# Performance work log

Hardware: AMD Instinct MI355X
Metric: run time of the kernel (lower is better)

Reference implementation:

```python
import jax, jax.numpy as jnp
import numpy as np

EPS = 1e-05


def setup_inputs() -> dict:
    key = jax.random.key(0)
    k1, k2, k3 = jax.random.split(key, 3)
    b, s, n, m = 16, 4096, 1024, 1024
    x = jax.random.normal(k1, (b, s, n), dtype=jnp.float32)
    # torch.rand -> uniform [0,1)
    A = jax.random.uniform(k2, (m, n), dtype=jnp.float32)
    B = jax.random.uniform(k3, (m, n), dtype=jnp.float32)
    return {"x": x, "A": A, "B": B}


def reference(x, A, B):
    # query: project each token with A, then sum over seq -> [b, m]
    query = jnp.einsum('ij,bsj->bi', A, x)  # fused projection + seq-sum
    query = query / (EPS + jnp.linalg.norm(query, axis=1, keepdims=True))
    # keys: [b, s, m], L2-normalized per token
    keys = jnp.einsum('ij,bsj->bsi', B, x)
    keys = keys / (EPS + jnp.linalg.norm(keys, axis=2, keepdims=True))
    # cosine-style similarity (no softmax): [b, s]
    sim = jnp.einsum('bi,bsi->bs', query, keys)
    # weighted sum of raw inputs: [b, n]
    out = jnp.einsum('bs,bsn->bn', sim, x)
    return (out, sim)
```

## Files before the change

kernel.cpp:

```cpp
#include <hip/hip_runtime.h>

#define EPS 1e-5f

typedef __bf16 bf16x8 __attribute__((ext_vector_type(8)));
typedef __bf16 bf16x4 __attribute__((ext_vector_type(4)));
typedef __bf16 bf16x2 __attribute__((ext_vector_type(2)));
typedef float f32x4 __attribute__((ext_vector_type(4)));

static __device__ __forceinline__ unsigned int f2bf(float f) {
    unsigned int u = __builtin_bit_cast(unsigned int, f);
    u = (u + 0x7fffu + ((u >> 16) & 1u)) >> 16;
    return u;
}

static __device__ __forceinline__ void gll16(const void* g, void* l) {
    __builtin_amdgcn_global_load_lds(
        (const __attribute__((address_space(1))) unsigned int*)(unsigned long long)g,
        (__attribute__((address_space(3))) unsigned int*)(unsigned int)(unsigned long long)l,
        16, 0, 0);
}

template <int XBF>
__global__ __launch_bounds__(256) void k_prep(const float* __restrict__ x,
                                              float* __restrict__ xs_part,
                                              unsigned short* __restrict__ xbf) {
    const int b = blockIdx.y, sc = blockIdx.x, tid = threadIdx.x;
    const size_t rowbase = ((size_t)(b * 4096 + sc * 128)) * 1024;
    const float4* src = (const float4*)(x + rowbase) + tid;
    uint2* dst = XBF ? ((uint2*)(xbf + rowbase) + tid) : (uint2*)0;
    float ax = 0.f, ay = 0.f, az = 0.f, aw = 0.f;
    for (int r = 0; r < 128; ++r) {
        float4 v = src[r * 256];
        ax += v.x; ay += v.y; az += v.z; aw += v.w;
        if (XBF) {
            uint2 p;
            p.x = f2bf(v.x) | (f2bf(v.y) << 16);
            p.y = f2bf(v.z) | (f2bf(v.w) << 16);
            dst[r * 256] = p;
        }
    }
    float4 o; o.x = ax; o.y = ay; o.z = az; o.w = aw;
    ((float4*)(xs_part + ((size_t)(b * 32 + sc)) * 1024))[tid] = o;
}

__global__ void k_bconv(const float* __restrict__ B, unsigned short* __restrict__ Bb) {
    const int i = blockIdx.x * 256 + threadIdx.x;
    float4 v = ((const float4*)B)[i];
    uint2 p;
    p.x = f2bf(v.x) | (f2bf(v.y) << 16);
    p.y = f2bf(v.z) | (f2bf(v.w) << 16);
    ((uint2*)Bb)[i] = p;
}

__global__ __launch_bounds__(256) void k_queryf(const float* __restrict__ xs_part,
                                                const float* __restrict__ A,
                                                float* __restrict__ q) {
    __shared__ float xsl[1024];
    const int b = blockIdx.y, g = blockIdx.x, tid = threadIdx.x;
    {
        float4 s4 = {0.f, 0.f, 0.f, 0.f};
        const float4* p = (const float4*)(xs_part + (size_t)b * 32768) + tid;
        for (int sc = 0; sc < 32; ++sc) {
            float4 v = p[sc * 256];
            s4.x += v.x; s4.y += v.y; s4.z += v.z; s4.w += v.w;
        }
        ((float4*)xsl)[tid] = s4;
    }
    __syncthreads();
    const int i = g * 256 + tid;
    const float4* ar = (const float4*)(A + (size_t)i * 1024);
    float acc = 0.f;
    for (int k = 0; k < 256; ++k) {
        float4 a = ar[k], v = ((const float4*)xsl)[k];
        acc += a.x * v.x + a.y * v.y + a.z * v.z + a.w * v.w;
    }
    q[b * 1024 + i] = acc;
}

__global__ __launch_bounds__(256) void k_wf(const float* __restrict__ B,
                                            const float* __restrict__ q,
                                            float* __restrict__ w) {
    __shared__ float ql[1024];
    __shared__ float wsum[4];
    const int b = blockIdx.y, g = blockIdx.x, tid = threadIdx.x;
    float4 v = ((const float4*)(q + (size_t)b * 1024))[tid];
    float ss = v.x * v.x + v.y * v.y + v.z * v.z + v.w * v.w;
    for (int o = 1; o < 64; o <<= 1) ss += __shfl_xor(ss, o);
    if ((tid & 63) == 0) wsum[tid >> 6] = ss;
    __syncthreads();
    const float inv = 1.f / (EPS + sqrtf(wsum[0] + wsum[1] + wsum[2] + wsum[3]));
    float4 n; n.x = v.x * inv; n.y = v.y * inv; n.z = v.z * inv; n.w = v.w * inv;
    ((float4*)ql)[tid] = n;
    __syncthreads();
    const int j = g * 256 + tid;
    float acc = 0.f;
    for (int i = 0; i < 1024; ++i) acc += B[(size_t)i * 1024 + j] * ql[i];
    w[b * 1024 + j] = acc;
}

__global__ __launch_bounds__(512, 2) void k_main2(const unsigned short* __restrict__ xbf,
                                                  const unsigned short* __restrict__ Bb,
                                                  const float* __restrict__ w,
                                                  float* __restrict__ outp,
                                                  float* __restrict__ sim_out) {
    __shared__ __align__(16) union {
        struct { unsigned short Xs[2][256 * 64]; unsigned short Bs[2][256 * 64]; } g;
        unsigned short xt2[2][32 * 1024];
    } S;
    __shared__ float nsq_s[256];
    __shared__ float wlds[1024];
    __shared__ float numer_s[32];
    __shared__ float simv[32];

    const int tid = threadIdx.x;
    const int lane = tid & 63;
    const int l15 = lane & 15, lg = lane >> 4;
    const int w8 = tid >> 6;
    const int wm = w8 >> 2, wn = w8 & 3;
    const int bx = blockIdx.x;
    const size_t tok0 = (size_t)bx * 256;
    const int b = bx >> 4;

    ((float2*)wlds)[tid] = ((const float2*)(w + (size_t)b * 1024))[tid];
    if (tid < 256) nsq_s[tid] = 0.f;
    __syncthreads();

#define STAGE(s_, buf_)                                                                  \
    do {                                                                                 \
        const int mt_ = (s_) >> 4, ks_ = (s_) & 15;                                      \
        _Pragma("unroll") for (int it = 0; it < 4; ++it) {                               \
            const int g_ = it * 512 + tid;                                               \
            const int row_ = g_ >> 3, c_ = g_ & 7;                                       \
            const int csw_ = (c_ ^ (row_ & 7)) * 8;                                      \
            gll16(xbf + (tok0 + row_) * 1024 + ks_ * 64 + csw_,                          \
                  (char*)S.g.Xs[buf_] + (size_t)(it * 512 + (tid & ~63)) * 16);          \
            gll16(Bb + (size_t)(mt_ * 256 + row_) * 1024 + ks_ * 64 + csw_,              \
                  (char*)S.g.Bs[buf_] + (size_t)(it * 512 + (tid & ~63)) * 16);          \
        }                                                                                \
    } while (0)

    f32x4 acc[8][4];

    STAGE(0, 0);
    STAGE(1, 1);

    for (int s = 0; s < 64; ++s) {
        const int buf = s & 1;
        if ((s & 15) == 0) {
#pragma unroll
            for (int mi = 0; mi < 8; ++mi)
#pragma unroll
                for (int ni = 0; ni < 4; ++ni) acc[mi][ni] = (f32x4){0.f, 0.f, 0.f, 0.f};
        }
        if (s < 62) asm volatile("s_waitcnt vmcnt(8)" ::: "memory");
        else        asm volatile("s_waitcnt vmcnt(0)" ::: "memory");
        __builtin_amdgcn_s_barrier();

        const char* xb = (const char*)S.g.Xs[buf] + (wm * 128 + l15) * 128;
        const char* bb = (const char*)S.g.Bs[buf] + (wn * 64 + l15) * 128;
        const int sw = (l15 & 7) << 4;

        bf16x8 bq[4][2];
#pragma unroll
        for (int ni = 0; ni < 4; ++ni)
#pragma unroll
            for (int kk = 0; kk < 2; ++kk)
                bq[ni][kk] = *(const bf16x8*)(bb + ni * 16 * 128 + ((kk * 64 + lg * 16) ^ sw));

        __builtin_amdgcn_s_setprio(1);
#pragma unroll
        for (int p = 0; p < 4; ++p) {
            bf16x8 a[2][2];
#pragma unroll
            for (int mi = 0; mi < 2; ++mi)
#pragma unroll
                for (int kk = 0; kk < 2; ++kk)
                    a[mi][kk] = *(const bf16x8*)(xb + (p * 2 + mi) * 16 * 128 +
                                                 ((kk * 64 + lg * 16) ^ sw));
#pragma unroll
            for (int mi = 0; mi < 2; ++mi)
#pragma unroll
                for (int ni = 0; ni < 4; ++ni)
#pragma unroll
                    for (int kk = 0; kk < 2; ++kk)
                        acc[p * 2 + mi][ni] = __builtin_amdgcn_mfma_f32_16x16x32_bf16(
                            a[mi][kk], bq[ni][kk], acc[p * 2 + mi][ni], 0, 0, 0);
        }
        __builtin_amdgcn_s_setprio(0);

        asm volatile("" ::: "memory");
        __builtin_amdgcn_s_barrier();
        asm volatile("" ::: "memory");
        if (s + 2 < 64) STAGE(s + 2, buf);

        if ((s & 15) == 15) {
#pragma unroll
            for (int mi = 0; mi < 8; ++mi)
#pragma unroll
                for (int r = 0; r < 4; ++r) {
                    float v = 0.f;
#pragma unroll
                    for (int ni = 0; ni < 4; ++ni) v += acc[mi][ni][r] * acc[mi][ni][r];
                    v += __shfl_xor(v, 1);
                    v += __shfl_xor(v, 2);
                    v += __shfl_xor(v, 4);
                    v += __shfl_xor(v, 8);
                    if (l15 == 0) atomicAdd(&nsq_s[wm * 128 + mi * 16 + lg * 4 + r], v);
                }
        }
    }
#undef STAGE

#define STAGE_SUB(sub_, bf_)                                                             \
    do {                                                                                 \
        _Pragma("unroll") for (int it = 0; it < 8; ++it) {                               \
            const int idx_ = it * 512 + tid;                                             \
            const int row_ = idx_ >> 7, c_ = idx_ & 127;                                 \
            gll16(xbf + (tok0 + (sub_) * 32 + row_) * 1024 + ((c_ ^ (row_ & 7)) * 8),    \
                  (char*)S.xt2[bf_] + (size_t)(it * 512 + (tid & ~63)) * 16);            \
        }                                                                                \
    } while (0)

    STAGE_SUB(0, 0);
    asm volatile("s_waitcnt lgkmcnt(0)" ::: "memory");
    __builtin_amdgcn_s_barrier();

    float oa0 = 0.f, oa1 = 0.f;
    for (int sub = 0; sub < 8; ++sub) {
        const int cur = sub & 1;
        if (sub < 7) STAGE_SUB(sub + 1, cur ^ 1);
        if (sub < 7) asm volatile("s_waitcnt vmcnt(8)" ::: "memory");
        else         asm volatile("s_waitcnt vmcnt(0)" ::: "memory");
        __builtin_amdgcn_s_barrier();

        const char* xt = (const char*)S.xt2[cur];
        {
            const int t = tid >> 4, kp = tid & 15;
            const char* pt = xt + t * 2048;
            const int sw2 = (t & 7) << 4;
            float acc2 = 0.f;
#pragma unroll
            for (int j = 0; j < 8; ++j) {
                bf16x8 v = *(const bf16x8*)(pt + ((j * 256 + kp * 16) ^ sw2));
                const float* wp = wlds + j * 128 + kp * 8;
#pragma unroll
                for (int e = 0; e < 8; ++e) acc2 += (float)v[e] * wp[e];
            }
            acc2 += __shfl_xor(acc2, 1);
            acc2 += __shfl_xor(acc2, 2);
            acc2 += __shfl_xor(acc2, 4);
            acc2 += __shfl_xor(acc2, 8);
            if (kp == 0) numer_s[t] = acc2;
        }
        asm volatile("s_waitcnt lgkmcnt(0)" ::: "memory");
        __builtin_amdgcn_s_barrier();

        if (tid < 32) {
            float sv = numer_s[tid] / (EPS + sqrtf(nsq_s[sub * 32 + tid]));
            simv[tid] = sv;
            sim_out[tok0 + sub * 32 + tid] = sv;
        }
        asm volatile("s_waitcnt lgkmcnt(0)" ::: "memory");
        __builtin_amdgcn_s_barrier();

        {
            const int nb = tid * 4;
#pragma unroll 4
            for (int t = 0; t < 32; ++t) {
                bf16x2 v = *(const bf16x2*)(xt + t * 2048 + (nb ^ ((t & 7) << 4)));
                float sv = simv[t];
                oa0 += sv * (float)v[0];
                oa1 += sv * (float)v[1];
            }
        }
        asm volatile("s_waitcnt lgkmcnt(0)" ::: "memory");
        __builtin_amdgcn_s_barrier();
    }
#undef STAGE_SUB
    float2 o; o.x = oa0; o.y = oa1;
    ((float2*)(outp + (size_t)bx * 1024))[tid] = o;
}

__global__ __launch_bounds__(256, 2) void k_nsq_f32(const float* __restrict__ x,
                                                    const unsigned short* __restrict__ Bb,
                                                    float* __restrict__ nsq_g) {
    __shared__ unsigned short Xs[128 * 64];
    __shared__ unsigned short Bs[128 * 64];
    __shared__ float nsq_s[128];

    const int tid = threadIdx.x;
    const int lane = tid & 63;
    const int l15 = lane & 15, lg = lane >> 4;
    const int w = tid >> 6;
    const int wr = w >> 1, wc = w & 1;
    const int st = blockIdx.x * 128;
    const int mh = blockIdx.y;

    float nsq_reg[4][4];
#pragma unroll
    for (int mi = 0; mi < 4; ++mi)
#pragma unroll
        for (int r = 0; r < 4; ++r) nsq_reg[mi][r] = 0.f;

    for (int mti = 0; mti < 4; ++mti) {
        const int mt = mh * 4 + mti;
        f32x4 acc[4][4];
#pragma unroll
        for (int mi = 0; mi < 4; ++mi)
#pragma unroll
            for (int ni = 0; ni < 4; ++ni) acc[mi][ni] = (f32x4){0.f, 0.f, 0.f, 0.f};

        for (int ks = 0; ks < 16; ++ks) {
            __syncthreads();
            {
                const int row = tid >> 1, kh = tid & 1;
                const float* srcx = x + (size_t)(st + row) * 1024 + ks * 64 + kh * 32;
                char* ldsrow = (char*)Xs + row * 128;
                const int sw = (row & 7) << 4;
#pragma unroll
                for (int j = 0; j < 4; ++j) {
                    float4 v0 = ((const float4*)srcx)[j * 2];
                    float4 v1 = ((const float4*)srcx)[j * 2 + 1];
                    uint4 p;
                    p.x = f2bf(v0.x) | (f2bf(v0.y) << 16);
                    p.y = f2bf(v0.z) | (f2bf(v0.w) << 16);
                    p.z = f2bf(v1.x) | (f2bf(v1.y) << 16);
                    p.w = f2bf(v1.z) | (f2bf(v1.w) << 16);
                    *(uint4*)(ldsrow + (((kh * 4 + j) * 16) ^ sw)) = p;
                }
#pragma unroll
                for (int it = 0; it < 4; ++it) {
                    const int idx = it * 256 + tid;
                    const int brow = idx >> 3, c = idx & 7;
                    char* baseB = (char*)Bs + (size_t)(it * 256 + (tid & ~63)) * 16;
                    gll16(Bb + (size_t)(mt * 128 + brow) * 1024 + ks * 64 + (c ^ (brow & 7)) * 8,
                          baseB);
                }
            }
            __syncthreads();

            const char* xb = (const char*)Xs + (wr * 64 + l15) * 128;
            const char* bb = (const char*)Bs + (wc * 64 + l15) * 128;
            const int sw = (l15 & 7) << 4;
#pragma unroll
            for (int kk = 0; kk < 2; ++kk) {
                const int ob = (kk * 64 + lg * 16) ^ sw;
                bf16x8 a[4], bq[4];
#pragma unroll
                for (int mi = 0; mi < 4; ++mi) a[mi] = *(const bf16x8*)(xb + mi * 2048 + ob);
#pragma unroll
                for (int ni = 0; ni < 4; ++ni) bq[ni] = *(const bf16x8*)(bb + ni * 2048 + ob);
#pragma unroll
                for (int mi = 0; mi < 4; ++mi)
#pragma unroll
                    for (int ni = 0; ni < 4; ++ni)
                        acc[mi][ni] = __builtin_amdgcn_mfma_f32_16x16x32_bf16(
                            a[mi], bq[ni], acc[mi][ni], 0, 0, 0);
            }
        }
#pragma unroll
        for (int mi = 0; mi < 4; ++mi)
#pragma unroll
            for (int ni = 0; ni < 4; ++ni)
#pragma unroll
                for (int r = 0; r < 4; ++r)
                    nsq_reg[mi][r] += acc[mi][ni][r] * acc[mi][ni][r];
    }

    if (tid < 128) nsq_s[tid] = 0.f;
    __syncthreads();
#pragma unroll
    for (int mi = 0; mi < 4; ++mi)
#pragma unroll
        for (int r = 0; r < 4; ++r) {
            float v = nsq_reg[mi][r];
            v += __shfl_xor(v, 1);
            v += __shfl_xor(v, 2);
            v += __shfl_xor(v, 4);
            v += __shfl_xor(v, 8);
            if (l15 == 0) atomicAdd(&nsq_s[wr * 64 + mi * 16 + lg * 4 + r], v);
        }
    __syncthreads();
    if (tid < 128) nsq_g[(size_t)mh * 65536 + st + tid] = nsq_s[tid];
}

__global__ __launch_bounds__(256, 2) void k_finish0(
    const float* __restrict__ x, const float* __restrict__ w,
    const float* __restrict__ nsq_g, float* __restrict__ outp,
    float* __restrict__ sim_out) {
    __shared__ __align__(16) unsigned short xt[32 * 1024];
    __shared__ float numer[32];
    __shared__ float simv[32];

    const int tid = threadIdx.x;
    const int bs = blockIdx.x;
    const int b = bs >> 7, s0 = (bs & 127) * 32;
    const size_t tok0 = (size_t)b * 4096 + s0;

    const float4* src = (const float4*)(x + tok0 * 1024) + tid;
    char* lds = (char*)xt;
    for (int r = 0; r < 32; ++r) {
        float4 v = src[r * 256];
        uint2 p;
        p.x = f2bf(v.x) | (f2bf(v.y) << 16);
        p.y = f2bf(v.z) | (f2bf(v.w) << 16);
        *(uint2*)(lds + r * 2048 + ((tid * 8) ^ ((r & 7) << 4))) = p;
    }
    __syncthreads();

    {
        const int t = tid >> 3, kp = tid & 7;
        const float* wb = w + (size_t)b * 1024 + kp * 128;
        const char* pt = (const char*)xt + t * 2048;
        const int sw2 = (t & 7) << 4;
        float acc = 0.f;
#pragma unroll
        for (int j = 0; j < 16; ++j) {
            const int kb = (kp * 128 + j * 8) * 2;
            bf16x8 v = *(const bf16x8*)(pt + (kb ^ sw2));
#pragma unroll
            for (int e = 0; e < 8; ++e) acc += (float)v[e] * wb[j * 8 + e];
        }
        acc += __shfl_xor(acc, 1);
        acc += __shfl_xor(acc, 2);
        acc += __shfl_xor(acc, 4);
        if (kp == 0) numer[t] = acc;
    }
    __syncthreads();

    if (tid < 32) {
        float nt = nsq_g[tok0 + tid] + nsq_g[65536 + tok0 + tid];
        float s = numer[tid] / (EPS + sqrtf(nt));
        simv[tid] = s;
        sim_out[tok0 + tid] = s;
    }
    __syncthreads();

    {
        const int n0 = tid * 4;
        float a0 = 0.f, a1 = 0.f, a2 = 0.f, a3 = 0.f;
        const char* p = (const char*)xt;
#pragma unroll 4
        for (int t = 0; t < 32; ++t) {
            int byte = t * 2048 + ((n0 * 2) ^ ((t & 7) << 4));
            bf16x4 v = *(const bf16x4*)(p + byte);
            float s = simv[t];
            a0 += s * (float)v[0];
            a1 += s * (float)v[1];
            a2 += s * (float)v[2];
            a3 += s * (float)v[3];
        }
        float4 o; o.x = a0; o.y = a1; o.z = a2; o.w = a3;
        ((float4*)(outp + (size_t)bs * 1024))[tid] = o;
    }
}

template <int NT>
__global__ void k_outred(const float* __restrict__ outp, float* __restrict__ out) {
    const int b = blockIdx.y, j = blockIdx.x * 256 + threadIdx.x;
    const float* p = outp + (size_t)b * NT * 1024 + j;
    float s = 0.f;
    for (int t = 0; t < NT; ++t) s += p[t * 1024];
    out[b * 1024 + j] = s;
}

extern "C" void kernel_launch(void* const* d_in, const int* in_sizes, int n_in,
                              void* d_out, int out_size, void* d_ws, size_t ws_size,
                              hipStream_t stream) {
    const float* x = (const float*)d_in[0];
    const float* A = (const float*)d_in[1];
    const float* B = (const float*)d_in[2];
    float* out = (float*)d_out;
    float* sim = out + 16 * 1024;
    float* ws = (float*)d_ws;
    float* xs_part = ws;
    float* q = ws + 540672;
    float* wv = ws + 557056;
    float* nsq = ws + 573440;
    float* outp = ws + 704512;
    unsigned short* Bb = (unsigned short*)(ws + 2801664);
    unsigned short* xbf = (unsigned short*)(ws + 3325952);
    const bool xb = ws_size >= (size_t)(3325952 + 33554432) * 4;

    if (xb) k_prep<1><<<dim3(32, 16), 256, 0, stream>>>(x, xs_part, xbf);
    else    k_prep<0><<<dim3(32, 16), 256, 0, stream>>>(x, xs_part, (unsigned short*)0);
    k_bconv<<<1024, 256, 0, stream>>>(B, Bb);
    k_queryf<<<dim3(4, 16), 256, 0, stream>>>(xs_part, A, q);
    k_wf<<<dim3(4, 16), 256, 0, stream>>>(B, q, wv);
    if (xb) {
        k_main2<<<256, 512, 0, stream>>>(xbf, Bb, wv, outp, sim);
        k_outred<16><<<dim3(4, 16), 256, 0, stream>>>(outp, out);
    } else {
        k_nsq_f32<<<dim3(512, 2), 256, 0, stream>>>(x, Bb, nsq);
        k_finish0<<<2048, 256, 0, stream>>>(x, wv, nsq, outp, sim);
        k_outred<128><<<dim3(4, 16), 256, 0, stream>>>(outp, out);
    }
}
```

Baseline: 303.8 us.

## Split GEMM K-tile into half-tiles with four-phase interleaved load/MFMA pipeline

Restructures the key-norm GEMM main loop so each 64-wide K tile is split into two 32-wide halves stored separately in LDS with a 4-way XOR swizzle. Each iteration now runs four MFMA phases, and each phase issues one quarter of the next global-to-LDS prefetch, with barriers and setprio placed around them. The aim is to spread global loads across the compute and hide latency better than one bulk stage per tile. It adds many more barriers per iteration, which may cost synchronization overhead. It also declares an unused nsq_reg array.

```diff
diff --git a/kernel.cpp b/kernel.cpp
--- a/kernel.cpp
+++ b/kernel.cpp
@@ -98,13 +98,15 @@
     w[b * 1024 + j] = acc;
 }
 
+#define FENCE asm volatile("" ::: "memory")
+
 __global__ __launch_bounds__(512, 2) void k_main2(const unsigned short* __restrict__ xbf,
                                                   const unsigned short* __restrict__ Bb,
                                                   const float* __restrict__ w,
                                                   float* __restrict__ outp,
                                                   float* __restrict__ sim_out) {
     __shared__ __align__(16) union {
-        struct { unsigned short Xs[2][256 * 64]; unsigned short Bs[2][256 * 64]; } g;
+        struct { unsigned short Xs[2][2][8192]; unsigned short Bs[2][2][8192]; } g;
         unsigned short xt2[2][32 * 1024];
     } S;
     __shared__ float nsq_s[256];
@@ -125,75 +127,115 @@
     if (tid < 256) nsq_s[tid] = 0.f;
     __syncthreads();
 
-#define STAGE(s_, buf_)                                                                  \
-    do {                                                                                 \
-        const int mt_ = (s_) >> 4, ks_ = (s_) & 15;                                      \
-        _Pragma("unroll") for (int it = 0; it < 4; ++it) {                               \
-            const int g_ = it * 512 + tid;                                               \
-            const int row_ = g_ >> 3, c_ = g_ & 7;                                       \
-            const int csw_ = (c_ ^ (row_ & 7)) * 8;                                      \
-            gll16(xbf + (tok0 + row_) * 1024 + ks_ * 64 + csw_,                          \
-                  (char*)S.g.Xs[buf_] + (size_t)(it * 512 + (tid & ~63)) * 16);          \
-            gll16(Bb + (size_t)(mt_ * 256 + row_) * 1024 + ks_ * 64 + csw_,              \
-                  (char*)S.g.Bs[buf_] + (size_t)(it * 512 + (tid & ~63)) * 16);          \
-        }                                                                                \
+#define STAGE_H(ts_, src_, lds_, kh_, rb_)                                              \
+    do {                                                                                \
+        const int ks_ = (ts_) & 15;                                                     \
+        _Pragma("unroll") for (int it_ = 0; it_ < 2; ++it_) {                           \
+            const int g_ = it_ * 512 + tid;                                             \
+            const int row_ = g_ >> 2, c2_ = g_ & 3;                                     \
+            const int cs_ = c2_ ^ (row_ & 3);                                           \
+            gll16((src_) + ((rb_) + row_) * 1024 + ks_ * 64 + (kh_) * 32 + cs_ * 8,     \
+                  (char*)(lds_) + (size_t)((kh_) * 1024 + it_ * 512 + (tid & ~63)) * 16); \
+        }                                                                               \
     } while (0)
 
+    const int sx = ((lg ^ (l15 & 3)) << 4);
+    const int aoff = (wm * 128 + l15) * 64 + sx;
+    const int boff = (wn * 64 + l15) * 64 + sx;
+
     f32x4 acc[8][4];
-
-    STAGE(0, 0);
-    STAGE(1, 1);
-
-    for (int s = 0; s < 64; ++s) {
-        const int buf = s & 1;
-        if ((s & 15) == 0) {
+    float nsq_reg[8][4];
+#pragma unroll
+    for (int mi = 0; mi < 8; ++mi)
+#pragma unroll
+        for (int r = 0; r < 4; ++r) nsq_reg[mi][r] = 0.f;
+
+    STAGE_H(0, xbf, S.g.Xs[0], 0, tok0);
+    STAGE_H(0, Bb,  S.g.Bs[0], 0, (size_t)0);
+    STAGE_H(0, xbf, S.g.Xs[0], 1, tok0);
+    STAGE_H(0, Bb,  S.g.Bs[0], 1, (size_t)0);
+    STAGE_H(1, xbf, S.g.Xs[1], 0, tok0);
+    STAGE_H(1, Bb,  S.g.Bs[1], 0, (size_t)0);
+    STAGE_H(1, xbf, S.g.Xs[1], 1, tok0);
+    asm volatile("s_waitcnt vmcnt(6)" ::: "memory");
+    __builtin_amdgcn_s_barrier();
+
+    for (int t = 0; t < 64; ++t) {
+        const int buf = t & 1;
+        if ((t & 15) == 0) {
 #pragma unroll
             for (int mi = 0; mi < 8; ++mi)
 #pragma unroll
                 for (int ni = 0; ni < 4; ++ni) acc[mi][ni] = (f32x4){0.f, 0.f, 0.f, 0.f};
         }
-        if (s < 62) asm volatile("s_waitcnt vmcnt(8)" ::: "memory");
+        const char* Xb = (const char*)S.g.Xs[buf];
+        const char* Bp = (const char*)S.g.Bs[buf];
+        bf16x8 a0[8], a1[8], bq0, bq1, bq2, bq3;
+
+#pragma unroll
+        for (int mi = 0; mi < 8; ++mi) a0[mi] = *(const bf16x8*)(Xb + mi * 1024 + aoff);
+        bq0 = *(const bf16x8*)(Bp + 0 * 1024 + boff);
+        bq1 = *(const bf16x8*)(Bp + 1 * 1024 + boff);
+        if (t < 63) STAGE_H(t + 1, Bb, S.g.Bs[buf ^ 1], 1, (size_t)(((t + 1) >> 4) * 256));
+        FENCE; __builtin_amdgcn_s_barrier();
+        asm volatile("s_waitcnt lgkmcnt(0)" ::: "memory");
+        __builtin_amdgcn_s_setprio(1);
+#pragma unroll
+        for (int mi = 0; mi < 8; ++mi) {
+            acc[mi][0] = __builtin_amdgcn_mfma_f32_16x16x32_bf16(a0[mi], bq0, acc[mi][0], 0, 0, 0);
+            acc[mi][1] = __builtin_amdgcn_mfma_f32_16x16x32_bf16(a0[mi], bq1, acc[mi][1], 0, 0, 0);
+        }
+        __builtin_amdgcn_s_setprio(0);
+        FENCE; __builtin_amdgcn_s_barrier();
+
+        bq2 = *(const bf16x8*)(Bp + 2 * 1024 + boff);
+        bq3 = *(const bf16x8*)(Bp + 3 * 1024 + boff);
+        if (t < 62) STAGE_H(t + 2, xbf, S.g.Xs[buf], 0, tok0);
+        FENCE; __builtin_amdgcn_s_barrier();
+        asm volatile("s_waitcnt lgkmcnt(0)" ::: "memory");
+        __builtin_amdgcn_s_setprio(1);
+#pragma unroll
+        for (int mi = 0; mi < 8; ++mi) {
+            acc[mi][2] = __builtin_amdgcn_mfma_f32_16x16x32_bf16(a0[mi], bq2, acc[mi][2], 0, 0, 0);
+            acc[mi][3] = __builtin_amdgcn_mfma_f32_16x16x32_bf16(a0[mi], bq3, acc[mi][3], 0, 0, 0);
+        }
+        __builtin_amdgcn_s_setprio(0);
+        FENCE; __builtin_amdgcn_s_barrier();
+
+#pragma unroll
+        for (int mi = 0; mi < 8; ++mi)
+            a1[mi] = *(const bf16x8*)(Xb + 16384 + mi * 1024 + aoff);
+        bq0 = *(const bf16x8*)(Bp + 16384 + 0 * 1024 + boff);
+        bq1 = *(const bf16x8*)(Bp + 16384 + 1 * 1024 + boff);
+        if (t < 62) STAGE_H(t + 2, Bb, S.g.Bs[buf], 0, (size_t)(((t + 2) >> 4) * 256));
+        FENCE; __builtin_amdgcn_s_barrier();
+        asm volatile("s_waitcnt lgkmcnt(0)" ::: "memory");
+        __builtin_amdgcn_s_setprio(1);
+#pragma unroll
+        for (int mi = 0; mi < 8; ++mi) {
+            acc[mi][0] = __builtin_amdgcn_mfma_f32_16x16x32_bf16(a1[mi], bq0, acc[mi][0], 0, 0, 0);
+            acc[mi][1] = __builtin_amdgcn_mfma_f32_16x16x32_bf16(a1[mi], bq1, acc[mi][1], 0, 0, 0);
+        }
+        __builtin_amdgcn_s_setprio(0);
+        FENCE; __builtin_amdgcn_s_barrier();
+
+        bq2 = *(const bf16x8*)(Bp + 16384 + 2 * 1024 + boff);
+        bq3 = *(const bf16x8*)(Bp + 16384 + 3 * 1024 + boff);
+        if (t < 62) STAGE_H(t + 2, xbf, S.g.Xs[buf], 1, tok0);
+        if (t < 62) asm volatile("s_waitcnt vmcnt(6)" ::: "memory");
         else        asm volatile("s_waitcnt vmcnt(0)" ::: "memory");
-        __builtin_amdgcn_s_barrier();
-
-        const char* xb = (const char*)S.g.Xs[buf] + (wm * 128 + l15) * 128;
-        const char* bb = (const char*)S.g.Bs[buf] + (wn * 64 + l15) * 128;
-        const int sw = (l15 & 7) << 4;
-
-        bf16x8 bq[4][2];
-#pragma unroll
-        for (int ni = 0; ni < 4; ++ni)
-#pragma unroll
-            for (int kk = 0; kk < 2; ++kk)
-                bq[ni][kk] = *(const bf16x8*)(bb + ni * 16 * 128 + ((kk * 64 + lg * 16) ^ sw));
-
+        FENCE; __builtin_amdgcn_s_barrier();
+        asm volatile("s_waitcnt lgkmcnt(0)" ::: "memory");
         __builtin_amdgcn_s_setprio(1);
 #pragma unroll
-        for (int p = 0; p < 4; ++p) {
-            bf16x8 a[2][2];
-#pragma unroll
-            for (int mi = 0; mi < 2; ++mi)
-#pragma unroll
-                for (int kk = 0; kk < 2; ++kk)
-                    a[mi][kk] = *(const bf16x8*)(xb + (p * 2 + mi) * 16 * 128 +
-                                                 ((kk * 64 + lg * 16) ^ sw));
-#pragma unroll
-            for (int mi = 0; mi < 2; ++mi)
-#pragma unroll
-                for (int ni = 0; ni < 4; ++ni)
-#pragma unroll
-                    for (int kk = 0; kk < 2; ++kk)
-                        acc[p * 2 + mi][ni] = __builtin_amdgcn_mfma_f32_16x16x32_bf16(
-                            a[mi][kk], bq[ni][kk], acc[p * 2 + mi][ni], 0, 0, 0);
+        for (int mi = 0; mi < 8; ++mi) {
+            acc[mi][2] = __builtin_amdgcn_mfma_f32_16x16x32_bf16(a1[mi], bq2, acc[mi][2], 0, 0, 0);
+            acc[mi][3] = __builtin_amdgcn_mfma_f32_16x16x32_bf16(a1[mi], bq3, acc[mi][3], 0, 0, 0);
         }
         __builtin_amdgcn_s_setprio(0);
-
-        asm volatile("" ::: "memory");
-        __builtin_amdgcn_s_barrier();
-        asm volatile("" ::: "memory");
-        if (s + 2 < 64) STAGE(s + 2, buf);
-
-        if ((s & 15) == 15) {
+        FENCE; __builtin_amdgcn_s_barrier();
+
+        if ((t & 15) == 15) {
 #pragma unroll
             for (int mi = 0; mi < 8; ++mi)
 #pragma unroll
@@ -209,7 +251,7 @@
                 }
         }
     }
-#undef STAGE
+#undef STAGE_H
 
 #define STAGE_SUB(sub_, bf_)                                                             \
     do {                                                                                 \
```

Result: slower. 315.9 us (+4.0%).

## Switch key GEMM to 32x32x16 MFMA tiles and transpose w layout in LDS

Applied to the files above, without the earlier changes.

The per-wave key projection now uses 32x32x16 bf16 MFMA instructions with 4x2 tiles of 16-wide accumulators, replacing 16x16x32 with 8x4 tiles. This cuts the LDS fragment reads per MFMA and the instruction count, and the row-norm reduction is remapped to the 32x32 output layout with an extra shuffle. Separately, the w vector is stored in LDS in a transposed order so the sim dot-product reads are conflict-free across kp lanes. The new accumulator layout carries a risk of register pressure and of mapping mistakes in the norm indices.

```diff
diff --git a/kernel.cpp b/kernel.cpp
--- a/kernel.cpp
+++ b/kernel.cpp
@@ -6,6 +6,7 @@
 typedef __bf16 bf16x4 __attribute__((ext_vector_type(4)));
 typedef __bf16 bf16x2 __attribute__((ext_vector_type(2)));
 typedef float f32x4 __attribute__((ext_vector_type(4)));
+typedef float f32x16 __attribute__((ext_vector_type(16)));
 
 static __device__ __forceinline__ unsigned int f2bf(float f) {
     unsigned int u = __builtin_bit_cast(unsigned int, f);
@@ -98,6 +99,8 @@
     w[b * 1024 + j] = acc;
 }
 
+#define FENCE asm volatile("" ::: "memory")
+
 __global__ __launch_bounds__(512, 2) void k_main2(const unsigned short* __restrict__ xbf,
                                                   const unsigned short* __restrict__ Bb,
                                                   const float* __restrict__ w,
@@ -114,14 +117,19 @@
 
     const int tid = threadIdx.x;
     const int lane = tid & 63;
-    const int l15 = lane & 15, lg = lane >> 4;
+    const int l31 = lane & 31, hi = lane >> 5;
     const int w8 = tid >> 6;
     const int wm = w8 >> 2, wn = w8 & 3;
     const int bx = blockIdx.x;
     const size_t tok0 = (size_t)bx * 256;
     const int b = bx >> 4;
 
-    ((float2*)wlds)[tid] = ((const float2*)(w + (size_t)b * 1024))[tid];
+    {
+        float2 wv2 = ((const float2*)(w + (size_t)b * 1024))[tid];
+        const int k0 = 2 * tid, k1 = 2 * tid + 1;
+        wlds[(((k0 & 7) + 8 * (k0 >> 7)) << 4) + ((k0 >> 3) & 15)] = wv2.x;
+        wlds[(((k1 & 7) + 8 * (k1 >> 7)) << 4) + ((k1 >> 3) & 15)] = wv2.y;
+    }
     if (tid < 256) nsq_s[tid] = 0.f;
     __syncthreads();
 
@@ -139,7 +147,7 @@
         }                                                                                \
     } while (0)
 
-    f32x4 acc[8][4];
+    f32x16 acc[4][2];
 
     STAGE(0, 0);
     STAGE(1, 1);
@@ -148,64 +156,62 @@
         const int buf = s & 1;
         if ((s & 15) == 0) {
 #pragma unroll
-            for (int mi = 0; mi < 8; ++mi)
-#pragma unroll
-                for (int ni = 0; ni < 4; ++ni) acc[mi][ni] = (f32x4){0.f, 0.f, 0.f, 0.f};
+            for (int mi = 0; mi < 4; ++mi)
+#pragma unroll
+                for (int ni = 0; ni < 2; ++ni)
+#pragma unroll
+                    for (int r = 0; r < 16; ++r) acc[mi][ni][r] = 0.f;
         }
         if (s < 62) asm volatile("s_waitcnt vmcnt(8)" ::: "memory");
         else        asm volatile("s_waitcnt vmcnt(0)" ::: "memory");
         __builtin_amdgcn_s_barrier();
 
-        const char* xb = (const char*)S.g.Xs[buf] + (wm * 128 + l15) * 128;
-        const char* bb = (const char*)S.g.Bs[buf] + (wn * 64 + l15) * 128;
-        const int sw = (l15 & 7) << 4;
-
-        bf16x8 bq[4][2];
-#pragma unroll
-        for (int ni = 0; ni < 4; ++ni)
-#pragma unroll
-            for (int kk = 0; kk < 2; ++kk)
-                bq[ni][kk] = *(const bf16x8*)(bb + ni * 16 * 128 + ((kk * 64 + lg * 16) ^ sw));
+        const char* xb = (const char*)S.g.Xs[buf] + (wm * 128 + l31) * 128;
+        const char* bb = (const char*)S.g.Bs[buf] + (wn * 64 + l31) * 128;
+        const int swz = (l31 & 7) << 4;
+
+        bf16x8 bq[2][4];
+#pragma unroll
+        for (int ni = 0; ni < 2; ++ni)
+#pragma unroll
+            for (int kk = 0; kk < 4; ++kk)
+                bq[ni][kk] = *(const bf16x8*)(bb + ni * 32 * 128 +
+                                              ((kk * 32 + hi * 16) ^ swz));
 
         __builtin_amdgcn_s_setprio(1);
 #pragma unroll
-        for (int p = 0; p < 4; ++p) {
-            bf16x8 a[2][2];
-#pragma unroll
-            for (int mi = 0; mi < 2; ++mi)
-#pragma unroll
-                for (int kk = 0; kk < 2; ++kk)
-                    a[mi][kk] = *(const bf16x8*)(xb + (p * 2 + mi) * 16 * 128 +
-                                                 ((kk * 64 + lg * 16) ^ sw));
-#pragma unroll
-            for (int mi = 0; mi < 2; ++mi)
-#pragma unroll
-                for (int ni = 0; ni < 4; ++ni)
-#pragma unroll
-                    for (int kk = 0; kk < 2; ++kk)
-                        acc[p * 2 + mi][ni] = __builtin_amdgcn_mfma_f32_16x16x32_bf16(
-                            a[mi][kk], bq[ni][kk], acc[p * 2 + mi][ni], 0, 0, 0);
+        for (int kk = 0; kk < 4; ++kk) {
+            bf16x8 a[4];
+#pragma unroll
+            for (int mi = 0; mi < 4; ++mi)
+                a[mi] = *(const bf16x8*)(xb + mi * 32 * 128 + ((kk * 32 + hi * 16) ^ swz));
+#pragma unroll
+            for (int mi = 0; mi < 4; ++mi)
+#pragma unroll
+                for (int ni = 0; ni < 2; ++ni)
+                    acc[mi][ni] = __builtin_amdgcn_mfma_f32_32x32x16_bf16(
+                        a[mi], bq[ni][kk], acc[mi][ni], 0, 0, 0);
         }
         __builtin_amdgcn_s_setprio(0);
 
-        asm volatile("" ::: "memory");
+        FENCE;
         __builtin_amdgcn_s_barrier();
-        asm volatile("" ::: "memory");
+        FENCE;
         if (s + 2 < 64) STAGE(s + 2, buf);
 
         if ((s & 15) == 15) {
 #pragma unroll
-            for (int mi = 0; mi < 8; ++mi)
-#pragma unroll
-                for (int r = 0; r < 4; ++r) {
-                    float v = 0.f;
-#pragma unroll
-                    for (int ni = 0; ni < 4; ++ni) v += acc[mi][ni][r] * acc[mi][ni][r];
+            for (int mi = 0; mi < 4; ++mi)
+#pragma unroll
+                for (int r = 0; r < 16; ++r) {
+                    float v = acc[mi][0][r] * acc[mi][0][r] + acc[mi][1][r] * acc[mi][1][r];
                     v += __shfl_xor(v, 1);
                     v += __shfl_xor(v, 2);
                     v += __shfl_xor(v, 4);
                     v += __shfl_xor(v, 8);
-                    if (l15 == 0) atomicAdd(&nsq_s[wm * 128 + mi * 16 + lg * 4 + r], v);
+                    v += __shfl_xor(v, 16);
+                    if (l31 == 0)
+                        atomicAdd(&nsq_s[wm * 128 + mi * 32 + (r & 3) + 8 * (r >> 2) + 4 * hi], v);
                 }
         }
     }
@@ -242,9 +248,9 @@
 #pragma unroll
             for (int j = 0; j < 8; ++j) {
                 bf16x8 v = *(const bf16x8*)(pt + ((j * 256 + kp * 16) ^ sw2));
-                const float* wp = wlds + j * 128 + kp * 8;
-#pragma unroll
-                for (int e = 0; e < 8; ++e) acc2 += (float)v[e] * wp[e];
+#pragma unroll
+                for (int e = 0; e < 8; ++e)
+                    acc2 += (float)v[e] * wlds[((j * 8 + e) << 4) + kp];
             }
             acc2 += __shfl_xor(acc2, 1);
             acc2 += __shfl_xor(acc2, 2);
```

New measurement: 336.5 us. +10.8%, slower.

## Fuse numerator into GEMM loop, merge glue kernels, atomically reduce output

Applied to the files above, without the earlier changes.

The numerator dot product x·w is now computed inside the main GEMM k-loop during the first 16 k-steps, reusing the X tile already staged in LDS, so the separate sub-tile pass no longer re-stages x. The weighted output sum reads bf16 x directly from global memory and accumulates into the final output with atomics. This removes the k_outred launch and the outp buffer, but needs a memset of the output. The B conversion and query kernels are merged into one launch to cut launch overhead. The trade-off is extra global reads of x in the epilogue and atomic contention across 16 blocks per batch.

```diff
diff --git a/kernel.cpp b/kernel.cpp
--- a/kernel.cpp
+++ b/kernel.cpp
@@ -4,13 +4,16 @@
 
 typedef __bf16 bf16x8 __attribute__((ext_vector_type(8)));
 typedef __bf16 bf16x4 __attribute__((ext_vector_type(4)));
-typedef __bf16 bf16x2 __attribute__((ext_vector_type(2)));
 typedef float f32x4 __attribute__((ext_vector_type(4)));
 
 static __device__ __forceinline__ unsigned int f2bf(float f) {
     unsigned int u = __builtin_bit_cast(unsigned int, f);
     u = (u + 0x7fffu + ((u >> 16) & 1u)) >> 16;
     return u;
+}
+static __device__ __forceinline__ float bf2f(unsigned int lo16) {
+    unsigned int u = lo16 << 16;
+    return __builtin_bit_cast(float, u);
 }
 
 static __device__ __forceinline__ void gll16(const void* g, void* l) {
@@ -43,20 +46,24 @@
     ((float4*)(xs_part + ((size_t)(b * 32 + sc)) * 1024))[tid] = o;
 }
 
-__global__ void k_bconv(const float* __restrict__ B, unsigned short* __restrict__ Bb) {
-    const int i = blockIdx.x * 256 + threadIdx.x;
-    float4 v = ((const float4*)B)[i];
-    uint2 p;
-    p.x = f2bf(v.x) | (f2bf(v.y) << 16);
-    p.y = f2bf(v.z) | (f2bf(v.w) << 16);
-    ((uint2*)Bb)[i] = p;
-}
-
-__global__ __launch_bounds__(256) void k_queryf(const float* __restrict__ xs_part,
-                                                const float* __restrict__ A,
-                                                float* __restrict__ q) {
+__global__ __launch_bounds__(256) void k_glue(const float* __restrict__ B,
+                                              unsigned short* __restrict__ Bb,
+                                              const float* __restrict__ xs_part,
+                                              const float* __restrict__ A,
+                                              float* __restrict__ q) {
     __shared__ float xsl[1024];
-    const int b = blockIdx.y, g = blockIdx.x, tid = threadIdx.x;
+    const int blk = blockIdx.x, tid = threadIdx.x;
+    if (blk < 1024) {
+        const int i = blk * 256 + tid;
+        float4 v = ((const float4*)B)[i];
+        uint2 p;
+        p.x = f2bf(v.x) | (f2bf(v.y) << 16);
+        p.y = f2bf(v.z) | (f2bf(v.w) << 16);
+        ((uint2*)Bb)[i] = p;
+        return;
+    }
+    const int gb = blk - 1024;
+    const int g = gb & 3, b = gb >> 2;
     {
         float4 s4 = {0.f, 0.f, 0.f, 0.f};
         const float4* p = (const float4*)(xs_part + (size_t)b * 32768) + tid;
@@ -98,19 +105,19 @@
     w[b * 1024 + j] = acc;
 }
 
+#define FENCE asm volatile("" ::: "memory")
+
 __global__ __launch_bounds__(512, 2) void k_main2(const unsigned short* __restrict__ xbf,
                                                   const unsigned short* __restrict__ Bb,
                                                   const float* __restrict__ w,
-                                                  float* __restrict__ outp,
+                                                  float* __restrict__ out,
                                                   float* __restrict__ sim_out) {
-    __shared__ __align__(16) union {
-        struct { unsigned short Xs[2][256 * 64]; unsigned short Bs[2][256 * 64]; } g;
-        unsigned short xt2[2][32 * 1024];
-    } S;
+    __shared__ __align__(16) unsigned short Xs[2][256 * 64];
+    __shared__ __align__(16) unsigned short Bs[2][256 * 64];
     __shared__ float nsq_s[256];
+    __shared__ float numer_s[256];
+    __shared__ float simv_s[256];
     __shared__ float wlds[1024];
-    __shared__ float numer_s[32];
-    __shared__ float simv[32];
 
     const int tid = threadIdx.x;
     const int lane = tid & 63;
@@ -133,13 +140,16 @@
             const int row_ = g_ >> 3, c_ = g_ & 7;                                       \
             const int csw_ = (c_ ^ (row_ & 7)) * 8;                                      \
             gll16(xbf + (tok0 + row_) * 1024 + ks_ * 64 + csw_,                          \
-                  (char*)S.g.Xs[buf_] + (size_t)(it * 512 + (tid & ~63)) * 16);          \
+                  (char*)Xs[buf_] + (size_t)(it * 512 + (tid & ~63)) * 16);              \
             gll16(Bb + (size_t)(mt_ * 256 + row_) * 1024 + ks_ * 64 + csw_,              \
-                  (char*)S.g.Bs[buf_] + (size_t)(it * 512 + (tid & ~63)) * 16);          \
+                  (char*)Bs[buf_] + (size_t)(it * 512 + (tid & ~63)) * 16);              \
         }                                                                                \
     } while (0)
 
     f32x4 acc[8][4];
+    float numer_acc = 0.f;
+    const int ntok = tid >> 1, nhalf = tid & 1;
+    const int nswt = (ntok & 7) << 4;
 
     STAGE(0, 0);
     STAGE(1, 1);
@@ -156,8 +166,8 @@
         else        asm volatile("s_waitcnt vmcnt(0)" ::: "memory");
         __builtin_amdgcn_s_barrier();
 
-        const char* xb = (const char*)S.g.Xs[buf] + (wm * 128 + l15) * 128;
-        const char* bb = (const char*)S.g.Bs[buf] + (wn * 64 + l15) * 128;
+        const char* xb = (const char*)Xs[buf] + (wm * 128 + l15) * 128;
+        const char* bb = (const char*)Bs[buf] + (wn * 64 + l15) * 128;
         const int sw = (l15 & 7) << 4;
 
         bf16x8 bq[4][2];
@@ -188,9 +198,22 @@
         }
         __builtin_amdgcn_s_setprio(0);
 
-        asm volatile("" ::: "memory");
+        if (s < 16) {
+            const char* pt = (const char*)Xs[buf] + ntok * 128;
+            const float* wp = wlds + s * 64 + nhalf * 32;
+            float na = 0.f;
+#pragma unroll
+            for (int j = 0; j < 4; ++j) {
+                bf16x8 v = *(const bf16x8*)(pt + ((nhalf * 64 + j * 16) ^ nswt));
+#pragma unroll
+                for (int e = 0; e < 8; ++e) na += (float)v[e] * wp[j * 8 + e];
+            }
+            numer_acc += na;
+        }
+
+        FENCE;
         __builtin_amdgcn_s_barrier();
-        asm volatile("" ::: "memory");
+        FENCE;
         if (s + 2 < 64) STAGE(s + 2, buf);
 
         if ((s & 15) == 15) {
@@ -208,77 +231,35 @@
                     if (l15 == 0) atomicAdd(&nsq_s[wm * 128 + mi * 16 + lg * 4 + r], v);
                 }
         }
+        if (s == 15) {
+            float na = numer_acc + __shfl_xor(numer_acc, 1);
+            if (nhalf == 0) numer_s[ntok] = na;
+        }
     }
 #undef STAGE
 
-#define STAGE_SUB(sub_, bf_)                                                             \
-    do {                                                                                 \
-        _Pragma("unroll") for (int it = 0; it < 8; ++it) {                               \
-            const int idx_ = it * 512 + tid;                                             \
-            const int row_ = idx_ >> 7, c_ = idx_ & 127;                                 \
-            gll16(xbf + (tok0 + (sub_) * 32 + row_) * 1024 + ((c_ ^ (row_ & 7)) * 8),    \
-                  (char*)S.xt2[bf_] + (size_t)(it * 512 + (tid & ~63)) * 16);            \
-        }                                                                                \
-    } while (0)
-
-    STAGE_SUB(0, 0);
-    asm volatile("s_waitcnt lgkmcnt(0)" ::: "memory");
-    __builtin_amdgcn_s_barrier();
-
-    float oa0 = 0.f, oa1 = 0.f;
-    for (int sub = 0; sub < 8; ++sub) {
-        const int cur = sub & 1;
-        if (sub < 7) STAGE_SUB(sub + 1, cur ^ 1);
-        if (sub < 7) asm volatile("s_waitcnt vmcnt(8)" ::: "memory");
-        else         asm volatile("s_waitcnt vmcnt(0)" ::: "memory");
-        __builtin_amdgcn_s_barrier();
-
-        const char* xt = (const char*)S.xt2[cur];
-        {
-            const int t = tid >> 4, kp = tid & 15;
-            const char* pt = xt + t * 2048;
-            const int sw2 = (t & 7) << 4;
-            float acc2 = 0.f;
-#pragma unroll
-            for (int j = 0; j < 8; ++j) {
-                bf16x8 v = *(const bf16x8*)(pt + ((j * 256 + kp * 16) ^ sw2));
-                const float* wp = wlds + j * 128 + kp * 8;
-#pragma unroll
-                for (int e = 0; e < 8; ++e) acc2 += (float)v[e] * wp[e];
-            }
-            acc2 += __shfl_xor(acc2, 1);
-            acc2 += __shfl_xor(acc2, 2);
-            acc2 += __shfl_xor(acc2, 4);
-            acc2 += __shfl_xor(acc2, 8);
-            if (kp == 0) numer_s[t] = acc2;
-        }
-        asm volatile("s_waitcnt lgkmcnt(0)" ::: "memory");
-        __builtin_amdgcn_s_barrier();
-
-        if (tid < 32) {
-            float sv = numer_s[tid] / (EPS + sqrtf(nsq_s[sub * 32 + tid]));
-            simv[tid] = sv;
-            sim_out[tok0 + sub * 32 + tid] = sv;
-        }
-        asm volatile("s_waitcnt lgkmcnt(0)" ::: "memory");
-        __builtin_amdgcn_s_barrier();
-
-        {
-            const int nb = tid * 4;
-#pragma unroll 4
-            for (int t = 0; t < 32; ++t) {
-                bf16x2 v = *(const bf16x2*)(xt + t * 2048 + (nb ^ ((t & 7) << 4)));
-                float sv = simv[t];
-                oa0 += sv * (float)v[0];
-                oa1 += sv * (float)v[1];
-            }
-        }
-        asm volatile("s_waitcnt lgkmcnt(0)" ::: "memory");
-        __builtin_amdgcn_s_barrier();
-    }
-#undef STAGE_SUB
-    float2 o; o.x = oa0; o.y = oa1;
-    ((float2*)(outp + (size_t)bx * 1024))[tid] = o;
+    __syncthreads();
+    if (tid < 256) {
+        float sv = numer_s[tid] / (EPS + sqrtf(nsq_s[tid]));
+        simv_s[tid] = sv;
+        sim_out[tok0 + tid] = sv;
+    }
+    __syncthreads();
+
+    {
+        const unsigned short* xp = xbf + tok0 * 1024 + tid * 2;
+        float oa0 = 0.f, oa1 = 0.f;
+#pragma unroll 8
+        for (int t = 0; t < 256; ++t) {
+            unsigned int u = *(const unsigned int*)(xp + (size_t)t * 1024);
+            float sv = simv_s[t];
+            oa0 += sv * bf2f(u & 0xffffu);
+            oa1 += sv * bf2f(u >> 16);
+        }
+        float* dst = out + (size_t)b * 1024 + tid * 2;
+        atomicAdd(dst + 0, oa0);
+        atomicAdd(dst + 1, oa1);
+    }
 }
 
 __global__ __launch_bounds__(256, 2) void k_nsq_f32(const float* __restrict__ x,
@@ -482,15 +463,16 @@
     unsigned short* xbf = (unsigned short*)(ws + 3325952);
     const bool xb = ws_size >= (size_t)(3325952 + 33554432) * 4;
 
-    if (xb) k_prep<1><<<dim3(32, 16), 256, 0, stream>>>(x, xs_part, xbf);
-    else    k_prep<0><<<dim3(32, 16), 256, 0, stream>>>(x, xs_part, (unsigned short*)0);
-    k_bconv<<<1024, 256, 0, stream>>>(B, Bb);
-    k_queryf<<<dim3(4, 16), 256, 0, stream>>>(xs_part, A, q);
-    k_wf<<<dim3(4, 16), 256, 0, stream>>>(B, q, wv);
     if (xb) {
-        k_main2<<<256, 512, 0, stream>>>(xbf, Bb, wv, outp, sim);
-        k_outred<16><<<dim3(4, 16), 256, 0, stream>>>(outp, out);
+        hipMemsetAsync(d_out, 0, 16 * 1024 * sizeof(float), stream);
+        k_prep<1><<<dim3(32, 16), 256, 0, stream>>>(x, xs_part, xbf);
+        k_glue<<<1088, 256, 0, stream>>>(B, Bb, xs_part, A, q);
+        k_wf<<<dim3(4, 16), 256, 0, stream>>>(B, q, wv);
+        k_main2<<<256, 512, 0, stream>>>(xbf, Bb, wv, out, sim);
     } else {
+        k_prep<0><<<dim3(32, 16), 256, 0, stream>>>(x, xs_part, (unsigned short*)0);
+        k_glue<<<1088, 256, 0, stream>>>(B, Bb, xs_part, A, q);
+        k_wf<<<dim3(4, 16), 256, 0, stream>>>(B, q, wv);
         k_nsq_f32<<<dim3(512, 2), 256, 0, stream>>>(x, Bb, nsq);
         k_finish0<<<2048, 256, 0, stream>>>(x, wv, nsq, outp, sim);
         k_outred<128><<<dim3(4, 16), 256, 0, stream>>>(outp, out);
```

Measured after the change: 305.6 us. No clear change (+0.6%).
